# Optimization experiments

Hardware: AMD Instinct MI355X
Metric: run time of the kernel (lower is better)

## Reference

```python
import jax, jax.numpy as jnp
import numpy as np

B = 64          # graphs per batch
N_NODES = 2000  # nodes per graph (model hyperparameter: FC2 in_features)
NF = 128        # node features
H = 8           # hidden_dim
OC = 8          # out_channels
NC = 2          # n_classes
DEG = 16        # avg degree
SLOPE = 0.01


def _lin_init(key, fan_in, fan_out):
    k1, k2 = jax.random.split(key)
    s = 1.0 / np.sqrt(fan_in)
    W = jax.random.uniform(k1, (fan_in, fan_out), jnp.float32, -s, s)
    b = jax.random.uniform(k2, (fan_out,), jnp.float32, -s, s)
    return W, b


def setup_inputs() -> dict:
    key = jax.random.key(0)
    ks = jax.random.split(key, 10)
    N = B * N_NODES
    E = N * DEG
    x = jax.random.normal(ks[0], (N, NF), jnp.float32)
    # graph-local random edges, offset per graph
    local = jax.random.randint(ks[1], (2, E), 0, N_NODES)
    off = jnp.repeat(jnp.arange(B, dtype=jnp.int64) * N_NODES, E // B)
    edge_index = (local + off[None, :]).astype(jnp.int64)
    batch = jnp.repeat(jnp.arange(B, dtype=jnp.int64), N_NODES)
    W1a, b1a = _lin_init(ks[2], NF, H)
    W1b, b1b = _lin_init(ks[3], H, H)
    W2a, b2a = _lin_init(ks[4], H, H)
    W2b, b2b = _lin_init(ks[5], H, OC)
    Wf1, bf1 = _lin_init(ks[6], OC, 1)
    Wf2, bf2 = _lin_init(ks[7], N_NODES, NC)
    return {"x": x, "edge_index": edge_index, "batch": batch,
            "W1a": W1a, "b1a": b1a, "W1b": W1b, "b1b": b1b,
            "W2a": W2a, "b2a": b2a, "W2b": W2b, "b2b": b2b,
            "Wf1": Wf1, "bf1": bf1, "Wf2": Wf2, "bf2": bf2}


def _lrelu(v):
    return jnp.where(v >= 0, v, SLOPE * v)


def _gin_conv(h, src, dst, Wa, ba, Wb, bb):
    N = h.shape[0]
    agg = jax.ops.segment_sum(h[src], dst, num_segments=N)  # sum_{j->i} h_j
    z = h + agg                                             # (1+eps)*h + agg, eps=0
    z = _lrelu(z @ Wa + ba)                                 # MLP linear1 + act
    return z @ Wb + bb                                      # MLP linear2 (plain last)


def reference(x, edge_index, batch, W1a, b1a, W1b, b1b, W2a, b2a, W2b, b2b,
              Wf1, bf1, Wf2, bf2):
    src, dst = edge_index[0], edge_index[1]
    h = _gin_conv(x, src, dst, W1a, b1a, W1b, b1b)
    h = _lrelu(h)  # inter-layer activation (dropout = identity at eval)
    h = _gin_conv(h, src, dst, W2a, b2a, W2b, b2b)  # [N, OC], no act after last conv
    bsz = h.shape[0] // N_NODES
    y = h.reshape(bsz, N_NODES, OC)
    y = _lrelu(y) @ Wf1 + bf1          # FC1 -> [B, n_nodes, 1]
    y = y.reshape(bsz, N_NODES)
    y = _lrelu(y) @ Wf2 + bf2          # FC2 -> [B, n_classes]
    return jax.nn.log_softmax(y, axis=1)
```

## Files before the change

### kernel.cpp

```cpp
#include <hip/hip_runtime.h>
#include <math.h>

#define NF 128
#define HD 8
#define NPG 2000
#define EPB 8000
#define LPB 8
#define LNPB 250
#define FNPB 128
#define SLOPE 0.01f

__device__ __forceinline__ float lrelu(float v) {
    return v > 0.0f ? v : SLOPE * v;
}
__device__ __forceinline__ unsigned short f2bf(float f) {
    unsigned int u = __float_as_uint(f);
    return (unsigned short)((u + 0x7FFFu + ((u >> 16) & 1u)) >> 16);
}
__device__ __forceinline__ float bfl(unsigned int p) {
    return __uint_as_float(p << 16);
}
__device__ __forceinline__ float bfh(unsigned int p) {
    return __uint_as_float(p & 0xFFFF0000u);
}
__device__ __forceinline__ void gload_lds16(const void* g, void* l) {
    __builtin_amdgcn_global_load_lds(
        (const __attribute__((address_space(1))) unsigned int*)g,
        (__attribute__((address_space(3))) unsigned int*)l, 16, 0, 0);
}

__global__ __launch_bounds__(1024) void k_featsort(
    const float* __restrict__ x, const float* __restrict__ W1a,
    const int* __restrict__ ei, unsigned short* __restrict__ t1b,
    unsigned short* __restrict__ gcolb, int* __restrict__ rpc,
    int N, int E, int NC)
{
    __shared__ union {
        struct { float tile[FNPB * NF]; float wl[8 * 132]; } f;
        struct { int cnt[NPG]; unsigned int pck[EPB]; int srt[EPB];
                 int wtot[16]; int wpre[16]; } s;
    } sm;

    const int tid = threadIdx.x;

    if ((int)blockIdx.x < NC) {
        const int b = blockIdx.x;
        const int g = b >> 2;
        const int lane = tid & 63;
        const int wv = tid >> 6;
        const int nodeBase = g * NPG;
        const int e0 = b * EPB;

        for (int i = tid; i < NPG; i += 1024) sm.s.cnt[i] = 0;
        __syncthreads();

        for (int e = e0 + tid; e < e0 + EPB; e += 1024) {
            int src = ei[e] - nodeBase;
            int dl = ei[E + e] - nodeBase;
            sm.s.pck[e - e0] = ((unsigned int)dl << 11) | (unsigned int)src;
            atomicAdd(&sm.s.cnt[dl], 1);
        }
        __syncthreads();

        int c0 = 0, c1 = 0;
        if (tid < 1000) { c0 = sm.s.cnt[2 * tid]; c1 = sm.s.cnt[2 * tid + 1]; }
        int s = c0 + c1;
        int isc = s;
#pragma unroll
        for (int d = 1; d < 64; d <<= 1) {
            int o = __shfl_up(isc, d);
            if (lane >= d) isc += o;
        }
        if (lane == 63) sm.s.wtot[wv] = isc;
        __syncthreads();
        if (wv == 0) {
            int v = (lane < 16) ? sm.s.wtot[lane] : 0;
            int iv = v;
#pragma unroll
            for (int d = 1; d < 16; d <<= 1) {
                int o = __shfl_up(iv, d);
                if (lane >= d) iv += o;
            }
            if (lane < 16) sm.s.wpre[lane] = iv - v;
        }
        __syncthreads();
        int excl = isc - s + sm.s.wpre[wv];

        int* rpb = rpc + (size_t)b * (NPG + 1);
        if (tid < 1000) {
            sm.s.cnt[2 * tid]     = excl;
            sm.s.cnt[2 * tid + 1] = excl + c0;
            rpb[2 * tid]     = excl;
            rpb[2 * tid + 1] = excl + c0;
        }
        if (tid == 0) rpb[NPG] = EPB;
        __syncthreads();

        for (int i = tid; i < EPB; i += 1024) {
            unsigned int p = sm.s.pck[i];
            int dl = (int)(p >> 11);
            int src = (int)(p & 2047u);
            int pos = atomicAdd(&sm.s.cnt[dl], 1);
            sm.s.srt[pos] = src;
        }
        __syncthreads();

        unsigned int* dst = (unsigned int*)(gcolb + (size_t)b * EPB);
        for (int i = tid; i < EPB / 2; i += 1024) {
            unsigned int lo = (unsigned int)sm.s.srt[2 * i] & 0xFFFFu;
            unsigned int hi = (unsigned int)sm.s.srt[2 * i + 1] << 16;
            dst[i] = lo | hi;
        }
    } else {
        const size_t base = (size_t)(blockIdx.x - NC) * FNPB;
        const int lane = tid & 63;
        const int wv6 = tid >> 6;

        {
            int wcol = tid >> 7;
            int wk   = tid & 127;
            sm.f.wl[wcol * 132 + wk] = W1a[wk * 8 + wcol];
        }

        const float* xg = x + base * NF;
        char* tb = (char*)sm.f.tile;
#pragma unroll
        for (int i = 0; i < 4; ++i) {
            int s = wv6 * 256 + i * 64 + lane;
            int n = s >> 5, j = s & 31;
            gload_lds16(xg + n * NF + ((j ^ (n & 7)) << 2), tb + s * 16);
        }
        __syncthreads();

        const int col   = tid & 7;
        const int khalf = (tid >> 3) & 1;
        const int np    = tid >> 4;
        const int n0    = np * 2;
        const int ex0 = n0 & 7, ex1 = (n0 + 1) & 7;

        const float*  tf = sm.f.tile;
        const float4* w4 = (const float4*)sm.f.wl;
        float acc0 = 0.0f, acc1 = 0.0f;
#pragma unroll 4
        for (int i = 0; i < 16; ++i) {
            int k4 = khalf * 16 + i;
            float4 r0 = *(const float4*)(tf + n0 * NF + ((k4 ^ ex0) << 2));
            float4 r1 = *(const float4*)(tf + (n0 + 1) * NF + ((k4 ^ ex1) << 2));
            float4 w  = w4[col * 33 + k4];
            acc0 += r0.x * w.x + r0.y * w.y + r0.z * w.z + r0.w * w.w;
            acc1 += r1.x * w.x + r1.y * w.y + r1.z * w.z + r1.w * w.w;
        }
        acc0 += __shfl_xor(acc0, 8);
        acc1 += __shfl_xor(acc1, 8);
        if (khalf == 0) {
            t1b[(base + n0) * HD + col]     = f2bf(acc0);
            t1b[(base + n0 + 1) * HD + col] = f2bf(acc1);
        }
    }
}

#define GATHER_CHUNK(P)                                                       \
    {                                                                         \
        int b0 = rs[P], cnt = re[P] - b0;                                     \
        int sl[8];                                                            \
        _Pragma("unroll")                                                     \
        for (int j = 0; j < 8; ++j) {                                         \
            int idx = (j < cnt) ? (b0 + j) : 0;                               \
            sl[j] = colp[P][idx];                                             \
        }                                                                     \
        _Pragma("unroll")                                                     \
        for (int j = 0; j < 8; ++j) {                                         \
            float w = (j < cnt) ? 1.0f : 0.0f;                                \
            uint4 v = tbl[sl[j]];                                             \
            a0 += w * bfl(v.x); a1 += w * bfh(v.x);                           \
            a2 += w * bfl(v.y); a3 += w * bfh(v.y);                           \
            a4 += w * bfl(v.z); a5 += w * bfh(v.z);                           \
            a6 += w * bfl(v.w); a7 += w * bfh(v.w);                           \
        }                                                                     \
        for (int e2 = b0 + 8; e2 < b0 + cnt; ++e2) {                          \
            uint4 v = tbl[colp[P][e2]];                                       \
            a0 += bfl(v.x); a1 += bfh(v.x);                                   \
            a2 += bfl(v.y); a3 += bfh(v.y);                                   \
            a4 += bfl(v.z); a5 += bfh(v.z);                                   \
            a6 += bfl(v.w); a7 += bfh(v.w);                                   \
        }                                                                     \
    }

__global__ __launch_bounds__(512) void k_l1(
    const unsigned short* __restrict__ t1b, const int* __restrict__ rpc,
    const unsigned short* __restrict__ gcolb, unsigned short* __restrict__ ub,
    const float* __restrict__ b1a, const float* __restrict__ W1b,
    const float* __restrict__ b1b, const float* __restrict__ W2a)
{
    __shared__ uint4 tbl[2048];
    __shared__ float wts[144];

    const int b = blockIdx.x;
    const int g = b >> 3;
    const int q = b & 7;
    const int tid = threadIdx.x;

    if (tid < 144) {
        float v;
        if (tid < 8)       v = b1a[tid];
        else if (tid < 72) v = W1b[tid - 8];
        else if (tid < 80) v = b1b[tid - 72];
        else               v = W2a[tid - 80];
        wts[tid] = v;
    }

    {
        const uint4* src4 = (const uint4*)(t1b + (size_t)g * NPG * HD);
        const int lane = tid & 63, w8 = tid >> 6;
        char* tb = (char*)tbl;
#pragma unroll
        for (int i = 0; i < 4; ++i) {
            int s = w8 * 256 + i * 64 + lane;
            gload_lds16(src4 + s, tb + s * 16);
        }
    }
    __syncthreads();

    if (tid < 2 * LNPB) {
        const int node = tid >> 1;
        const int half = tid & 1;
        const int nl = q * LNPB + node;
        int rs[2], re[2];
        const unsigned short* colp[2];
#pragma unroll
        for (int p = 0; p < 2; ++p) {
            int ch = half * 2 + p;
            const int* rpb = rpc + (size_t)((g << 2) + ch) * (NPG + 1);
            colp[p] = gcolb + (size_t)((g << 2) + ch) * EPB;
            rs[p] = rpb[nl]; re[p] = rpb[nl + 1];
        }
        float a0 = 0, a1 = 0, a2 = 0, a3 = 0, a4 = 0, a5 = 0, a6 = 0, a7 = 0;
        GATHER_CHUNK(0) GATHER_CHUNK(1)
        a0 += __shfl_xor(a0, 1); a1 += __shfl_xor(a1, 1);
        a2 += __shfl_xor(a2, 1); a3 += __shfl_xor(a3, 1);
        a4 += __shfl_xor(a4, 1); a5 += __shfl_xor(a5, 1);
        a6 += __shfl_xor(a6, 1); a7 += __shfl_xor(a7, 1);

        if (half == 0) {
            uint4 sv = tbl[nl];
            float z[HD];
            z[0] = lrelu(bfl(sv.x) + a0 + wts[0]); z[1] = lrelu(bfh(sv.x) + a1 + wts[1]);
            z[2] = lrelu(bfl(sv.y) + a2 + wts[2]); z[3] = lrelu(bfh(sv.y) + a3 + wts[3]);
            z[4] = lrelu(bfl(sv.z) + a4 + wts[4]); z[5] = lrelu(bfh(sv.z) + a5 + wts[5]);
            z[6] = lrelu(bfl(sv.w) + a6 + wts[6]); z[7] = lrelu(bfh(sv.w) + a7 + wts[7]);

            float h[HD];
#pragma unroll
            for (int j = 0; j < HD; ++j) {
                float acc = wts[72 + j];
#pragma unroll
                for (int c = 0; c < HD; ++c) acc += z[c] * wts[8 + c * HD + j];
                h[j] = lrelu(acc);
            }
            float uu[HD];
#pragma unroll
            for (int j = 0; j < HD; ++j) {
                float acc = 0.0f;
#pragma unroll
                for (int c = 0; c < HD; ++c) acc += h[c] * wts[80 + c * HD + j];
                uu[j] = acc;
            }
            uint4 pk;
            pk.x = (unsigned int)f2bf(uu[0]) | ((unsigned int)f2bf(uu[1]) << 16);
            pk.y = (unsigned int)f2bf(uu[2]) | ((unsigned int)f2bf(uu[3]) << 16);
            pk.z = (unsigned int)f2bf(uu[4]) | ((unsigned int)f2bf(uu[5]) << 16);
            pk.w = (unsigned int)f2bf(uu[6]) | ((unsigned int)f2bf(uu[7]) << 16);
            ((uint4*)ub)[(size_t)g * NPG + nl] = pk;
        }
    }
}

__global__ __launch_bounds__(512) void k_l2(
    const unsigned short* __restrict__ ub, const int* __restrict__ rpc,
    const unsigned short* __restrict__ gcolb,
    const float* __restrict__ b2a, const float* __restrict__ W2b,
    const float* __restrict__ b2b, const float* __restrict__ Wf1,
    const float* __restrict__ bf1, const float* __restrict__ Wf2,
    float* __restrict__ bparts)
{
    __shared__ uint4 tbl[2048];
    __shared__ float wts[89];
    __shared__ float red[16];

    const int b = blockIdx.x;
    const int g = b >> 3;
    const int q = b & 7;
    const int tid = threadIdx.x;
    const int lane = tid & 63;
    const int wv = tid >> 6;

    if (tid < 89) {
        float v;
        if (tid < 8)       v = b2a[tid];
        else if (tid < 72) v = W2b[tid - 8];
        else if (tid < 80) v = b2b[tid - 72];
        else if (tid < 88) v = Wf1[tid - 80];
        else               v = bf1[0];
        wts[tid] = v;
    }

    {
        const uint4* src4 = (const uint4*)(ub + (size_t)g * NPG * HD);
        char* tb = (char*)tbl;
#pragma unroll
        for (int i = 0; i < 4; ++i) {
            int s = wv * 256 + i * 64 + lane;
            gload_lds16(src4 + s, tb + s * 16);
        }
    }
    __syncthreads();

    float acc0 = 0.0f, acc1 = 0.0f;
    if (tid < 2 * LNPB) {
        const int node = tid >> 1;
        const int half = tid & 1;
        const int nl = q * LNPB + node;
        int rs[2], re[2];
        const unsigned short* colp[2];
#pragma unroll
        for (int p = 0; p < 2; ++p) {
            int ch = half * 2 + p;
            const int* rpb = rpc + (size_t)((g << 2) + ch) * (NPG + 1);
            colp[p] = gcolb + (size_t)((g << 2) + ch) * EPB;
            rs[p] = rpb[nl]; re[p] = rpb[nl + 1];
        }
        float a0 = 0, a1 = 0, a2 = 0, a3 = 0, a4 = 0, a5 = 0, a6 = 0, a7 = 0;
        GATHER_CHUNK(0) GATHER_CHUNK(1)
        a0 += __shfl_xor(a0, 1); a1 += __shfl_xor(a1, 1);
        a2 += __shfl_xor(a2, 1); a3 += __shfl_xor(a3, 1);
        a4 += __shfl_xor(a4, 1); a5 += __shfl_xor(a5, 1);
        a6 += __shfl_xor(a6, 1); a7 += __shfl_xor(a7, 1);

        if (half == 0) {
            uint4 sv = tbl[nl];
            float z[HD];
            z[0] = lrelu(bfl(sv.x) + a0 + wts[0]); z[1] = lrelu(bfh(sv.x) + a1 + wts[1]);
            z[2] = lrelu(bfl(sv.y) + a2 + wts[2]); z[3] = lrelu(bfh(sv.y) + a3 + wts[3]);
            z[4] = lrelu(bfl(sv.z) + a4 + wts[4]); z[5] = lrelu(bfh(sv.z) + a5 + wts[5]);
            z[6] = lrelu(bfl(sv.w) + a6 + wts[6]); z[7] = lrelu(bfh(sv.w) + a7 + wts[7]);

            float svl = wts[88];
#pragma unroll
            for (int j = 0; j < HD; ++j) {
                float acc = wts[72 + j];
#pragma unroll
                for (int c = 0; c < HD; ++c) acc += z[c] * wts[8 + c * HD + j];
                svl += lrelu(acc) * wts[80 + j];
            }
            float pf = lrelu(svl);
            float2 wf = *(const float2*)(Wf2 + (size_t)nl * 2);
            acc0 = pf * wf.x;
            acc1 = pf * wf.y;
        }
    }

#pragma unroll
    for (int off = 32; off > 0; off >>= 1) {
        acc0 += __shfl_down(acc0, off);
        acc1 += __shfl_down(acc1, off);
    }
    if (lane == 0) { red[wv * 2] = acc0; red[wv * 2 + 1] = acc1; }
    __syncthreads();

    if (tid == 0) {
        float y0 = 0.f, y1 = 0.f;
#pragma unroll
        for (int w = 0; w < 8; ++w) { y0 += red[w * 2]; y1 += red[w * 2 + 1]; }
        *(float2*)(bparts + (size_t)b * 2) = make_float2(y0, y1);
    }
}

__global__ __launch_bounds__(64) void k_fin(const float* __restrict__ bparts,
                                            const float* __restrict__ bf2,
                                            float* __restrict__ out, int Bn) {
    int g = threadIdx.x;
    if (g >= Bn) return;
    float y0 = bf2[0], y1 = bf2[1];
#pragma unroll
    for (int b = 0; b < LPB; ++b) {
        float2 v = *(const float2*)(bparts + (size_t)(g * LPB + b) * 2);
        y0 += v.x; y1 += v.y;
    }
    float m = fmaxf(y0, y1);
    float lse = m + logf(expf(y0 - m) + expf(y1 - m));
    out[g * 2 + 0] = y0 - lse;
    out[g * 2 + 1] = y1 - lse;
}

extern "C" void kernel_launch(void* const* d_in, const int* in_sizes, int n_in,
                              void* d_out, int out_size, void* d_ws, size_t ws_size,
                              hipStream_t stream) {
    const float* x   = (const float*)d_in[0];
    const int*   ei  = (const int*)  d_in[1];
    const float* W1a = (const float*)d_in[3];
    const float* b1a = (const float*)d_in[4];
    const float* W1b = (const float*)d_in[5];
    const float* b1b = (const float*)d_in[6];
    const float* W2a = (const float*)d_in[7];
    const float* b2a = (const float*)d_in[8];
    const float* W2b = (const float*)d_in[9];
    const float* b2b = (const float*)d_in[10];
    const float* Wf1 = (const float*)d_in[11];
    const float* bf1 = (const float*)d_in[12];
    const float* Wf2 = (const float*)d_in[13];
    const float* bf2 = (const float*)d_in[14];

    int N   = in_sizes[0] / NF;
    int E   = in_sizes[1] / 2;
    int Bn  = N / NPG;
    int NC  = Bn * 4;

    unsigned short* t1b   = (unsigned short*)d_ws;
    unsigned short* ubuf  = t1b + (size_t)N * HD;
    unsigned short* gcolb = ubuf + (size_t)N * HD;
    int*            rpc   = (int*)(gcolb + (size_t)E);
    float*          bparts= (float*)(rpc + (size_t)NC * (NPG + 1) + 16);

    k_featsort<<<NC + N / FNPB, 1024, 0, stream>>>(x, W1a, ei, t1b, gcolb, rpc,
                                                   N, E, NC);
    k_l1 <<<Bn * LPB, 512, 0, stream>>>(t1b, rpc, gcolb, ubuf, b1a, W1b, b1b, W2a);
    k_l2 <<<Bn * LPB, 512, 0, stream>>>(ubuf, rpc, gcolb, b2a, W2b, b2b, Wf1,
                                        bf1, Wf2, bparts);
    k_fin<<<1, 64, 0, stream>>>(bparts, bf2, (float*)d_out, Bn);
}
```

Before: 157.6 us.

## Compute first-layer projection one node per thread reading x directly

The feature projection x@W1a no longer stages x tiles in LDS. Each thread now handles one node, streams its 128-float row straight from global memory with float4 loads, and accumulates all 8 output columns against W1a broadcast from LDS. It writes one packed uint4 of bf16 values per node. This removes the LDS tile staging, the cross-lane shuffle reduction and the scalar stores, and each block now covers 1024 nodes instead of 128. In exchange each thread's loads are strided by a whole row, so coalescing across a wavefront is lost and the per-thread register count rises.

```diff
diff --git a/kernel.cpp b/kernel.cpp
--- a/kernel.cpp
+++ b/kernel.cpp
@@ -7,7 +7,7 @@
 #define EPB 8000
 #define LPB 8
 #define LNPB 250
-#define FNPB 128
+#define FNPB 1024
 #define SLOPE 0.01f
 
 __device__ __forceinline__ float lrelu(float v) {
@@ -29,14 +29,14 @@
         (__attribute__((address_space(3))) unsigned int*)l, 16, 0, 0);
 }
 
-__global__ __launch_bounds__(1024) void k_featsort(
+__global__ __launch_bounds__(1024, 8) void k_featsort(
     const float* __restrict__ x, const float* __restrict__ W1a,
     const int* __restrict__ ei, unsigned short* __restrict__ t1b,
     unsigned short* __restrict__ gcolb, int* __restrict__ rpc,
     int N, int E, int NC)
 {
     __shared__ union {
-        struct { float tile[FNPB * NF]; float wl[8 * 132]; } f;
+        struct { float wl[NF * HD]; } f;
         struct { int cnt[NPG]; unsigned int pck[EPB]; int srt[EPB];
                  int wtot[16]; int wpre[16]; } s;
     } sm;
@@ -113,49 +113,49 @@
         }
     } else {
         const size_t base = (size_t)(blockIdx.x - NC) * FNPB;
-        const int lane = tid & 63;
-        const int wv6 = tid >> 6;
-
-        {
-            int wcol = tid >> 7;
-            int wk   = tid & 127;
-            sm.f.wl[wcol * 132 + wk] = W1a[wk * 8 + wcol];
-        }
-
-        const float* xg = x + base * NF;
-        char* tb = (char*)sm.f.tile;
-#pragma unroll
-        for (int i = 0; i < 4; ++i) {
-            int s = wv6 * 256 + i * 64 + lane;
-            int n = s >> 5, j = s & 31;
-            gload_lds16(xg + n * NF + ((j ^ (n & 7)) << 2), tb + s * 16);
-        }
-        __syncthreads();
-
-        const int col   = tid & 7;
-        const int khalf = (tid >> 3) & 1;
-        const int np    = tid >> 4;
-        const int n0    = np * 2;
-        const int ex0 = n0 & 7, ex1 = (n0 + 1) & 7;
-
-        const float*  tf = sm.f.tile;
+        const int node = (int)base + tid;
+
+        sm.f.wl[tid] = W1a[tid];
+        __syncthreads();
+
+        const float4* xr = (const float4*)(x + (size_t)node * NF);
         const float4* w4 = (const float4*)sm.f.wl;
-        float acc0 = 0.0f, acc1 = 0.0f;
-#pragma unroll 4
-        for (int i = 0; i < 16; ++i) {
-            int k4 = khalf * 16 + i;
-            float4 r0 = *(const float4*)(tf + n0 * NF + ((k4 ^ ex0) << 2));
-            float4 r1 = *(const float4*)(tf + (n0 + 1) * NF + ((k4 ^ ex1) << 2));
-            float4 w  = w4[col * 33 + k4];
-            acc0 += r0.x * w.x + r0.y * w.y + r0.z * w.z + r0.w * w.w;
-            acc1 += r1.x * w.x + r1.y * w.y + r1.z * w.z + r1.w * w.w;
-        }
-        acc0 += __shfl_xor(acc0, 8);
-        acc1 += __shfl_xor(acc1, 8);
-        if (khalf == 0) {
-            t1b[(base + n0) * HD + col]     = f2bf(acc0);
-            t1b[(base + n0 + 1) * HD + col] = f2bf(acc1);
-        }
+        float accL[8] = {0, 0, 0, 0, 0, 0, 0, 0};
+        float accH[8] = {0, 0, 0, 0, 0, 0, 0, 0};
+
+#pragma unroll
+        for (int kb = 0; kb < 8; ++kb) {
+            float4 r[4];
+#pragma unroll
+            for (int j = 0; j < 4; ++j) r[j] = xr[kb * 4 + j];
+            float* acc = (kb < 4) ? accL : accH;
+#pragma unroll
+            for (int c4 = 0; c4 < 4; ++c4) {
+#pragma unroll
+                for (int e = 0; e < 4; ++e) {
+                    const int k = kb * 16 + c4 * 4 + e;
+                    const float xs = (e == 0) ? r[c4].x : (e == 1) ? r[c4].y
+                                   : (e == 2) ? r[c4].z : r[c4].w;
+                    float4 wA = w4[k * 2];
+                    float4 wB = w4[k * 2 + 1];
+                    acc[0] += xs * wA.x; acc[1] += xs * wA.y;
+                    acc[2] += xs * wA.z; acc[3] += xs * wA.w;
+                    acc[4] += xs * wB.x; acc[5] += xs * wB.y;
+                    acc[6] += xs * wB.z; acc[7] += xs * wB.w;
+                }
+            }
+        }
+
+        uint4 pk;
+        pk.x = (unsigned int)f2bf(accL[0] + accH[0]) |
+               ((unsigned int)f2bf(accL[1] + accH[1]) << 16);
+        pk.y = (unsigned int)f2bf(accL[2] + accH[2]) |
+               ((unsigned int)f2bf(accL[3] + accH[3]) << 16);
+        pk.z = (unsigned int)f2bf(accL[4] + accH[4]) |
+               ((unsigned int)f2bf(accL[5] + accH[5]) << 16);
+        pk.w = (unsigned int)f2bf(accL[6] + accH[6]) |
+               ((unsigned int)f2bf(accL[7] + accH[7]) << 16);
+        ((uint4*)t1b)[node] = pk;
     }
 }
 
@@ -199,6 +199,8 @@
     const int g = b >> 3;
     const int q = b & 7;
     const int tid = threadIdx.x;
+    const int lane = tid & 63;
+    const int wv = tid >> 6;
 
     if (tid < 144) {
         float v;
@@ -211,11 +213,10 @@
 
     {
         const uint4* src4 = (const uint4*)(t1b + (size_t)g * NPG * HD);
-        const int lane = tid & 63, w8 = tid >> 6;
         char* tb = (char*)tbl;
 #pragma unroll
         for (int i = 0; i < 4; ++i) {
-            int s = w8 * 256 + i * 64 + lane;
+            int s = wv * 256 + i * 64 + lane;
             gload_lds16(src4 + s, tb + s * 16);
         }
     }
```

New measurement: 175.9 us. 1.12x slower.

## Halve featsort block size and shrink shared memory for higher occupancy

Applied to the files above, without the earlier changes.

Reduces k_featsort from 1024 to 512 threads per block, with 64 nodes per feature block and a four-per-thread scan in the sort blocks. The sort path no longer stages packed edges in shared memory. It re-reads the edge list from global memory in the scatter pass and stores sorted sources as 16-bit values, which shrinks the LDS footprint. The aim is more resident blocks per CU and better latency hiding, at the cost of a second global read of edge indices and twice as many feature blocks.

```diff
diff --git a/kernel.cpp b/kernel.cpp
--- a/kernel.cpp
+++ b/kernel.cpp
@@ -7,7 +7,7 @@
 #define EPB 8000
 #define LPB 8
 #define LNPB 250
-#define FNPB 128
+#define FNPB 64
 #define SLOPE 0.01f
 
 __device__ __forceinline__ float lrelu(float v) {
@@ -29,7 +29,7 @@
         (__attribute__((address_space(3))) unsigned int*)l, 16, 0, 0);
 }
 
-__global__ __launch_bounds__(1024) void k_featsort(
+__global__ __launch_bounds__(512, 8) void k_featsort(
     const float* __restrict__ x, const float* __restrict__ W1a,
     const int* __restrict__ ei, unsigned short* __restrict__ t1b,
     unsigned short* __restrict__ gcolb, int* __restrict__ rpc,
@@ -37,34 +37,35 @@
 {
     __shared__ union {
         struct { float tile[FNPB * NF]; float wl[8 * 132]; } f;
-        struct { int cnt[NPG]; unsigned int pck[EPB]; int srt[EPB];
-                 int wtot[16]; int wpre[16]; } s;
+        struct { int cnt[NPG]; unsigned short srt[EPB];
+                 int wtot[8]; int wpre[8]; } s;
     } sm;
 
     const int tid = threadIdx.x;
+    const int lane = tid & 63;
+    const int wv = tid >> 6;
 
     if ((int)blockIdx.x < NC) {
         const int b = blockIdx.x;
         const int g = b >> 2;
-        const int lane = tid & 63;
-        const int wv = tid >> 6;
         const int nodeBase = g * NPG;
         const int e0 = b * EPB;
 
-        for (int i = tid; i < NPG; i += 1024) sm.s.cnt[i] = 0;
-        __syncthreads();
-
-        for (int e = e0 + tid; e < e0 + EPB; e += 1024) {
-            int src = ei[e] - nodeBase;
+        for (int i = tid; i < NPG; i += 512) sm.s.cnt[i] = 0;
+        __syncthreads();
+
+        for (int e = e0 + tid; e < e0 + EPB; e += 512) {
             int dl = ei[E + e] - nodeBase;
-            sm.s.pck[e - e0] = ((unsigned int)dl << 11) | (unsigned int)src;
             atomicAdd(&sm.s.cnt[dl], 1);
         }
         __syncthreads();
 
-        int c0 = 0, c1 = 0;
-        if (tid < 1000) { c0 = sm.s.cnt[2 * tid]; c1 = sm.s.cnt[2 * tid + 1]; }
-        int s = c0 + c1;
+        int c0 = 0, c1 = 0, c2 = 0, c3 = 0;
+        if (tid < 500) {
+            c0 = sm.s.cnt[4 * tid];     c1 = sm.s.cnt[4 * tid + 1];
+            c2 = sm.s.cnt[4 * tid + 2]; c3 = sm.s.cnt[4 * tid + 3];
+        }
+        int s = c0 + c1 + c2 + c3;
         int isc = s;
 #pragma unroll
         for (int d = 1; d < 64; d <<= 1) {
@@ -74,51 +75,48 @@
         if (lane == 63) sm.s.wtot[wv] = isc;
         __syncthreads();
         if (wv == 0) {
-            int v = (lane < 16) ? sm.s.wtot[lane] : 0;
+            int v = (lane < 8) ? sm.s.wtot[lane] : 0;
             int iv = v;
 #pragma unroll
-            for (int d = 1; d < 16; d <<= 1) {
+            for (int d = 1; d < 8; d <<= 1) {
                 int o = __shfl_up(iv, d);
                 if (lane >= d) iv += o;
             }
-            if (lane < 16) sm.s.wpre[lane] = iv - v;
+            if (lane < 8) sm.s.wpre[lane] = iv - v;
         }
         __syncthreads();
         int excl = isc - s + sm.s.wpre[wv];
 
         int* rpb = rpc + (size_t)b * (NPG + 1);
-        if (tid < 1000) {
-            sm.s.cnt[2 * tid]     = excl;
-            sm.s.cnt[2 * tid + 1] = excl + c0;
-            rpb[2 * tid]     = excl;
-            rpb[2 * tid + 1] = excl + c0;
+        if (tid < 500) {
+            int o0 = excl, o1 = excl + c0, o2 = o1 + c1, o3 = o2 + c2;
+            sm.s.cnt[4 * tid]     = o0; sm.s.cnt[4 * tid + 1] = o1;
+            sm.s.cnt[4 * tid + 2] = o2; sm.s.cnt[4 * tid + 3] = o3;
+            rpb[4 * tid]     = o0; rpb[4 * tid + 1] = o1;
+            rpb[4 * tid + 2] = o2; rpb[4 * tid + 3] = o3;
         }
         if (tid == 0) rpb[NPG] = EPB;
         __syncthreads();
 
-        for (int i = tid; i < EPB; i += 1024) {
-            unsigned int p = sm.s.pck[i];
-            int dl = (int)(p >> 11);
-            int src = (int)(p & 2047u);
+        for (int e = e0 + tid; e < e0 + EPB; e += 512) {
+            int src = ei[e] - nodeBase;
+            int dl = ei[E + e] - nodeBase;
             int pos = atomicAdd(&sm.s.cnt[dl], 1);
-            sm.s.srt[pos] = src;
+            sm.s.srt[pos] = (unsigned short)src;
         }
         __syncthreads();
 
         unsigned int* dst = (unsigned int*)(gcolb + (size_t)b * EPB);
-        for (int i = tid; i < EPB / 2; i += 1024) {
-            unsigned int lo = (unsigned int)sm.s.srt[2 * i] & 0xFFFFu;
-            unsigned int hi = (unsigned int)sm.s.srt[2 * i + 1] << 16;
-            dst[i] = lo | hi;
-        }
+        const unsigned int* ss = (const unsigned int*)sm.s.srt;
+        for (int i = tid; i < EPB / 2; i += 512) dst[i] = ss[i];
     } else {
         const size_t base = (size_t)(blockIdx.x - NC) * FNPB;
-        const int lane = tid & 63;
-        const int wv6 = tid >> 6;
-
-        {
-            int wcol = tid >> 7;
-            int wk   = tid & 127;
+
+#pragma unroll
+        for (int i = 0; i < 2; ++i) {
+            int idx = tid + i * 512;
+            int wcol = idx >> 7;
+            int wk   = idx & 127;
             sm.f.wl[wcol * 132 + wk] = W1a[wk * 8 + wcol];
         }
 
@@ -126,7 +124,7 @@
         char* tb = (char*)sm.f.tile;
 #pragma unroll
         for (int i = 0; i < 4; ++i) {
-            int s = wv6 * 256 + i * 64 + lane;
+            int s = wv * 256 + i * 64 + lane;
             int n = s >> 5, j = s & 31;
             gload_lds16(xg + n * NF + ((j ^ (n & 7)) << 2), tb + s * 16);
         }
@@ -199,6 +197,8 @@
     const int g = b >> 3;
     const int q = b & 7;
     const int tid = threadIdx.x;
+    const int lane = tid & 63;
+    const int wv = tid >> 6;
 
     if (tid < 144) {
         float v;
@@ -211,11 +211,10 @@
 
     {
         const uint4* src4 = (const uint4*)(t1b + (size_t)g * NPG * HD);
-        const int lane = tid & 63, w8 = tid >> 6;
         char* tb = (char*)tbl;
 #pragma unroll
         for (int i = 0; i < 4; ++i) {
-            int s = w8 * 256 + i * 64 + lane;
+            int s = wv * 256 + i * 64 + lane;
             gload_lds16(src4 + s, tb + s * 16);
         }
     }
@@ -421,8 +420,8 @@
     int*            rpc   = (int*)(gcolb + (size_t)E);
     float*          bparts= (float*)(rpc + (size_t)NC * (NPG + 1) + 16);
 
-    k_featsort<<<NC + N / FNPB, 1024, 0, stream>>>(x, W1a, ei, t1b, gcolb, rpc,
-                                                   N, E, NC);
+    k_featsort<<<NC + N / FNPB, 512, 0, stream>>>(x, W1a, ei, t1b, gcolb, rpc,
+                                                  N, E, NC);
     k_l1 <<<Bn * LPB, 512, 0, stream>>>(t1b, rpc, gcolb, ubuf, b1a, W1b, b1b, W2a);
     k_l2 <<<Bn * LPB, 512, 0, stream>>>(ubuf, rpc, gcolb, b2a, W2b, b2b, Wf1,
                                         bf1, Wf2, bparts);
```

New measurement: 152.6 us (median of 2 runs). 1.03x faster.
